# Kernel tuning notes

Measured on AMD Instinct MI355X. Metric: run time of the kernel, lower is better.

Reference implementation:

```python
import jax, jax.numpy as jnp
import numpy as np

B, L, D = 2, 2048, 1024
DH = 64
NH = D // DH
EPS = 1e-5
NEG = -1e30


def rms_norm(x, w):
    # x: (..., dh); norm in fp32 like the torch module, then scale by weight
    xf = x.astype(jnp.float32)
    y = xf * jax.lax.rsqrt(jnp.mean(xf * xf, axis=-1, keepdims=True) + EPS)
    return y.astype(x.dtype) * w.astype(x.dtype)


def sdpa(q, k, v, m):
    # q:(b,h,lq,dh) k,v:(b,h,lk,dh) m:(lq,lk) bool
    scale = 1.0 / jnp.sqrt(jnp.asarray(DH, q.dtype))
    s = jnp.einsum('bhqd,bhkd->bhqk', q, k) * scale
    s = jnp.where(m[None, None], s, NEG)
    p = jax.nn.softmax(s, axis=-1)
    return jnp.einsum('bhqk,bhkd->bhqd', p, v)


def setup_inputs() -> dict:
    key = jax.random.key(0)
    k1, k2, k3 = jax.random.split(key, 3)
    x = jax.random.normal(k1, (B, L, D), dtype=jnp.float32)
    mask = jnp.tril(jnp.ones((L, L), dtype=bool))  # causal: no fully-masked rows
    w_qkv = jax.random.normal(k2, (3 * D, D), dtype=jnp.float32) * (1.0 / np.sqrt(D))
    w_fc = jax.random.normal(k3, (D, D), dtype=jnp.float32) * (1.0 / np.sqrt(D))
    q_norm_w = jnp.ones((DH,), dtype=jnp.float32)
    k_norm_w = jnp.ones((DH,), dtype=jnp.float32)
    return {"x": x, "mask": mask, "w_qkv": w_qkv, "w_fc": w_fc,
            "q_norm_w": q_norm_w, "k_norm_w": k_norm_w,
            "subset_attention_size": 1024}


def reference(x, mask, w_qkv, w_fc, q_norm_w, k_norm_w, subset_attention_size):
    b, l, d = x.shape
    qkv = jnp.einsum('bld,ed->ble', x, w_qkv)  # (b,l,3d)
    q, k, v = jnp.split(qkv, 3, axis=-1)

    def heads(t):
        return t.reshape(b, l, NH, DH).transpose(0, 2, 1, 3)  # (b,nh,l,dh)

    q, k, v = heads(q), heads(k), heads(v)
    q = rms_norm(q, q_norm_w)
    k = rms_norm(k, k_norm_w)

    S = subset_attention_size
    if S is not None and S < l:
        o1 = sdpa(q[:, :, :S], k[:, :, :S], v[:, :, :S], mask[:S, :S])
        o2 = sdpa(q[:, :, S:], k, v, mask[S:, :])
        o = jnp.concatenate([o1, o2], axis=2)
    else:
        o = sdpa(q, k, v, mask)
    o = o.transpose(0, 2, 1, 3).reshape(b, l, d)  # (b,l,d)
    return jnp.einsum('bld,ed->ble', o, w_fc)
```

## Files before the change

### kernel.cpp

```cpp
#include <hip/hip_runtime.h>

typedef __bf16 bf16x8 __attribute__((ext_vector_type(8)));
typedef __bf16 bf16x4 __attribute__((ext_vector_type(4)));
typedef float f32x4 __attribute__((ext_vector_type(4)));
typedef short s16x4 __attribute__((ext_vector_type(4)));
typedef unsigned short u16;
typedef unsigned int u32;
typedef unsigned short u16x4 __attribute__((ext_vector_type(4)));
typedef unsigned short u16x8 __attribute__((ext_vector_type(8)));

#define AS1 __attribute__((address_space(1)))
#define AS3 __attribute__((address_space(3)))

__device__ __forceinline__ u16 f2bf(float f) {
  unsigned u = __builtin_bit_cast(unsigned, f);
  u += 0x7fffu + ((u >> 16) & 1u);
  return (u16)(u >> 16);
}

__device__ __forceinline__ float fast_exp2(float x) {
#if __has_builtin(__builtin_amdgcn_exp2f)
  return __builtin_amdgcn_exp2f(x);
#else
  return exp2f(x);
#endif
}

__device__ __forceinline__ f32x4 mfma16(s16x4 a, s16x4 b, f32x4 c) {
#if __has_builtin(__builtin_amdgcn_mfma_f32_16x16x16bf16_1k)
  return __builtin_amdgcn_mfma_f32_16x16x16bf16_1k(a, b, c, 0, 0, 0);
#else
  asm("v_mfma_f32_16x16x16_bf16 %0, %1, %2, %0" : "+v"(c) : "v"(a), "v"(b));
  return c;
#endif
}

__global__ __launch_bounds__(256) void cvt_all(const float* __restrict__ x,
                                               const float* __restrict__ wq,
                                               const float* __restrict__ wf,
                                               u16* __restrict__ xb, u16* __restrict__ wqb,
                                               u16* __restrict__ wfb) {
  long i = ((long)blockIdx.x * 256 + threadIdx.x) * 4;
  const float* src;
  u16* dst;
  long off;
  if (i < 4194304L) {
    src = x; dst = xb; off = i;
  } else if (i < 7340032L) {
    src = wq; dst = wqb; off = i - 4194304L;
  } else {
    src = wf; dst = wfb; off = i - 7340032L;
  }
  float4 v = *reinterpret_cast<const float4*>(src + off);
  u16x4 o;
  o.x = f2bf(v.x); o.y = f2bf(v.y); o.z = f2bf(v.z); o.w = f2bf(v.w);
  *reinterpret_cast<u16x4*>(dst + off) = o;
}

__global__ __launch_bounds__(256, 2) void gemm_qkv(const u16* __restrict__ A,
                                                   const u16* __restrict__ W,
                                                   u16* __restrict__ Qb,
                                                   u16* __restrict__ Kbf,
                                                   u16* __restrict__ vt,
                                                   const float* __restrict__ qw,
                                                   const float* __restrict__ kw) {
  constexpr int K = 1024;
  __shared__ __align__(16) u16 As[128 * 32];
  __shared__ __align__(16) u16 Bs[128 * 32];
  __shared__ __align__(16) u16 Ts[128 * 136];
  const int tid = threadIdx.x;
  const int lane = tid & 63;
  const int wid = tid >> 6;
  const int wm = wid >> 1, wn = wid & 1;
  const int l16 = lane & 15, g4 = lane >> 4;
  const long bm = blockIdx.x, bn = blockIdx.y;

  const int srow = tid >> 2;
  const int scol = (tid & 3) * 8;
  const u16* aA0 = A + (bm * 128 + srow) * (long)K + scol;
  const u16* aA1 = aA0 + 64 * (long)K;
  const u16* aW0 = W + (bn * 128 + srow) * (long)K + scol;
  const u16* aW1 = aW0 + 64 * (long)K;

  f32x4 acc[4][4] = {};

  for (int kt = 0; kt < K; kt += 32) {
    __builtin_amdgcn_global_load_lds((AS1 void*)(aA0 + kt), (AS3 void*)(&As[tid * 8]), 16, 0, 0);
    __builtin_amdgcn_global_load_lds((AS1 void*)(aA1 + kt), (AS3 void*)(&As[2048 + tid * 8]), 16, 0, 0);
    __builtin_amdgcn_global_load_lds((AS1 void*)(aW0 + kt), (AS3 void*)(&Bs[tid * 8]), 16, 0, 0);
    __builtin_amdgcn_global_load_lds((AS1 void*)(aW1 + kt), (AS3 void*)(&Bs[2048 + tid * 8]), 16, 0, 0);
    __syncthreads();
    bf16x8 af[4], bfr[4];
#pragma unroll
    for (int m = 0; m < 4; ++m)
      af[m] = *reinterpret_cast<const bf16x8*>(&As[(wm * 64 + m * 16 + l16) * 32 + g4 * 8]);
#pragma unroll
    for (int n = 0; n < 4; ++n)
      bfr[n] = *reinterpret_cast<const bf16x8*>(&Bs[(wn * 64 + n * 16 + l16) * 32 + g4 * 8]);
#pragma unroll
    for (int m = 0; m < 4; ++m)
#pragma unroll
      for (int n = 0; n < 4; ++n)
        acc[m][n] = __builtin_amdgcn_mfma_f32_16x16x32_bf16(af[m], bfr[n], acc[m][n], 0, 0, 0);
    __syncthreads();
  }

  if (bn < 16) {
    const float qscale = 0.18033688011112042f;
    const float* w = (bn < 8) ? qw : kw;
    const float ws = (bn < 8) ? qscale : 1.0f;
    float wv[4];
#pragma unroll
    for (int n = 0; n < 4; ++n) wv[n] = w[n * 16 + l16] * ws;
#pragma unroll
    for (int m = 0; m < 4; ++m) {
#pragma unroll
      for (int j = 0; j < 4; ++j) {
        float ss = 0.f;
#pragma unroll
        for (int n = 0; n < 4; ++n) ss = fmaf(acc[m][n][j], acc[m][n][j], ss);
        ss += __shfl_xor(ss, 1);
        ss += __shfl_xor(ss, 2);
        ss += __shfl_xor(ss, 4);
        ss += __shfl_xor(ss, 8);
        const float inv = rsqrtf(ss * (1.0f / 64.0f) + 1e-5f);
#pragma unroll
        for (int n = 0; n < 4; ++n) acc[m][n][j] *= inv * wv[n];
      }
    }
    u16* dst = (bn < 8) ? Qb : Kbf;
    const long cb = (bn < 8) ? bn : (bn - 8);
#pragma unroll
    for (int m = 0; m < 4; ++m)
#pragma unroll
      for (int n = 0; n < 4; ++n)
#pragma unroll
        for (int j = 0; j < 4; ++j) {
          long row = bm * 128 + wm * 64 + m * 16 + g4 * 4 + j;
          long col = cb * 128 + wn * 64 + n * 16 + l16;
          dst[row * 1024 + col] = f2bf(acc[m][n][j]);
        }
  } else {
#pragma unroll
    for (int m = 0; m < 4; ++m)
#pragma unroll
      for (int n = 0; n < 4; ++n) {
        bf16x4 w4;
#pragma unroll
        for (int j = 0; j < 4; ++j) w4[j] = (__bf16)acc[m][n][j];
        const int lc = wn * 64 + n * 16 + l16;
        const int lr = wm * 64 + m * 16 + g4 * 4;
        *reinterpret_cast<bf16x4*>(&Ts[lc * 136 + lr]) = w4;
      }
    __syncthreads();
    const int b = (int)(bm >> 4);
    const int keybase = ((int)(bm & 15)) * 128;
#pragma unroll
    for (int u = 0; u < 2; ++u) {
      const int unit = u * 256 + tid;
      const int hh = unit >> 8;
      const int d = (unit >> 2) & 63;
      const int kc = (unit & 3) * 32;
      const long bhv = b * 16 + (bn - 16) * 2 + hh;
      u16* dstp = vt + bhv * 131072L + (long)d * 2048 + keybase + kc;
      const u16* srcp = &Ts[(hh * 64 + d) * 136 + kc];
#pragma unroll
      for (int c = 0; c < 4; ++c)
        *reinterpret_cast<u16x8*>(dstp + c * 8) =
            *reinterpret_cast<const u16x8*>(srcp + c * 8);
    }
  }
}

__global__ __launch_bounds__(256, 2) void gemm_fc(const u16* __restrict__ A,
                                                  const u16* __restrict__ W,
                                                  float* __restrict__ C) {
  constexpr int N = 1024, K = 1024;
  __shared__ __align__(16) u16 As[128 * 32];
  __shared__ __align__(16) u16 Bs[64 * 32];
  const int tid = threadIdx.x;
  const int lane = tid & 63;
  const int wid = tid >> 6;
  const int wm = wid >> 1, wn = wid & 1;
  const int l16 = lane & 15, g4 = lane >> 4;
  const long bm = blockIdx.x, bn = blockIdx.y;

  const int srow = tid >> 2;
  const int scol = (tid & 3) * 8;
  const u16* aA0 = A + (bm * 128 + srow) * (long)K + scol;
  const u16* aA1 = aA0 + 64 * (long)K;
  const u16* aW0 = W + (bn * 64 + srow) * (long)K + scol;

  f32x4 acc[4][2] = {};

  for (int kt = 0; kt < K; kt += 32) {
    __builtin_amdgcn_global_load_lds((AS1 void*)(aA0 + kt), (AS3 void*)(&As[tid * 8]), 16, 0, 0);
    __builtin_amdgcn_global_load_lds((AS1 void*)(aA1 + kt), (AS3 void*)(&As[2048 + tid * 8]), 16, 0, 0);
    __builtin_amdgcn_global_load_lds((AS1 void*)(aW0 + kt), (AS3 void*)(&Bs[tid * 8]), 16, 0, 0);
    __syncthreads();
    bf16x8 af[4], bfr[2];
#pragma unroll
    for (int m = 0; m < 4; ++m)
      af[m] = *reinterpret_cast<const bf16x8*>(&As[(wm * 64 + m * 16 + l16) * 32 + g4 * 8]);
#pragma unroll
    for (int n = 0; n < 2; ++n)
      bfr[n] = *reinterpret_cast<const bf16x8*>(&Bs[(wn * 32 + n * 16 + l16) * 32 + g4 * 8]);
#pragma unroll
    for (int m = 0; m < 4; ++m)
#pragma unroll
      for (int n = 0; n < 2; ++n)
        acc[m][n] = __builtin_amdgcn_mfma_f32_16x16x32_bf16(af[m], bfr[n], acc[m][n], 0, 0, 0);
    __syncthreads();
  }

#pragma unroll
  for (int m = 0; m < 4; ++m)
#pragma unroll
    for (int n = 0; n < 2; ++n)
#pragma unroll
      for (int j = 0; j < 4; ++j) {
        long row = bm * 128 + wm * 64 + m * 16 + g4 * 4 + j;
        long col = bn * 64 + wn * 32 + n * 16 + l16;
        C[row * N + col] = acc[m][n][j];
      }
}

__global__ __launch_bounds__(256, 4) void attn_causal(const u16* __restrict__ Qb,
                                                      const u16* __restrict__ Kbf,
                                                      const u16* __restrict__ vt,
                                                      u16* __restrict__ o) {
  __shared__ __align__(16) u16 SMEM[16384];

  const int tid = threadIdx.x, lane = tid & 63, wid = tid >> 6;
  const int l16 = lane & 15, g4 = lane >> 4;
  const int h8 = (l16 & 7) << 4;
  const int qh = wid & 1, kh = wid >> 1;

  const int f = blockIdx.x;
  const int xcd = f & 7;
  const int g = f >> 3;
  const int hb = g >> 5;
  const int w = g & 31;
  const int bh = xcd * 4 + hb;
  const int basei = (w & 1) ? (31 - (w >> 1)) : (w >> 1);
  const int it = (hb & 1) ? (31 - basei) : basei;

  const long base = (long)(bh >> 4) * 2048 * 1024 + (bh & 15) * 64;
  const u16* qb = Qb + base;
  const u16* kb = Kbf + base;
  const u16* vtb = vt + (long)bh * 131072;

  bf16x8 qv[2][2];
#pragma unroll
  for (int qf = 0; qf < 2; ++qf) {
    const u16* qp = qb + ((long)it * 64 + qh * 32 + qf * 16 + l16) * 1024;
    qv[qf][0] = *reinterpret_cast<const bf16x8*>(qp + g4 * 8);
    qv[qf][1] = *reinterpret_cast<const bf16x8*>(qp + 32 + g4 * 8);
  }

  f32x4 acc[2][4] = {};
  f32x4 lacc[2] = {};

  s16x4 ones4;
#pragma unroll
  for (int j = 0; j < 4; ++j) ones4[j] = (short)0x3F80;

  const int krow = tid >> 3;
  const int scolE = (((tid & 7) * 16) ^ ((krow & 7) << 4)) >> 1;

  auto stage_issue = [&](int buf, int kt) {
    u16* KB = SMEM + buf * 4096;
    u16* VB = SMEM + 8192 + buf * 4096;
    __builtin_amdgcn_global_load_lds((AS1 void*)(kb + (long)(kt * 64 + krow) * 1024 + scolE),
                                     (AS3 void*)(&KB[tid * 8]), 16, 0, 0);
    __builtin_amdgcn_global_load_lds((AS1 void*)(kb + (long)(kt * 64 + krow + 32) * 1024 + scolE),
                                     (AS3 void*)(&KB[2048 + tid * 8]), 16, 0, 0);
    __builtin_amdgcn_global_load_lds((AS1 void*)(vtb + (long)krow * 2048 + kt * 64 + scolE),
                                     (AS3 void*)(&VB[tid * 8]), 16, 0, 0);
    __builtin_amdgcn_global_load_lds((AS1 void*)(vtb + (long)(krow + 32) * 2048 + kt * 64 + scolE),
                                     (AS3 void*)(&VB[2048 + tid * 8]), 16, 0, 0);
  };

  auto tile_step = [&](int cur, bool diag) {
    if (diag && qh == 0 && kh == 1) return;
    const u16* KB = SMEM + cur * 4096;
    const u16* VB = SMEM + 8192 + cur * 4096;
    bf16x8 kfr[2][2];
#pragma unroll
    for (int kf = 0; kf < 2; ++kf) {
      const int row = kh * 32 + kf * 16 + l16;
#pragma unroll
      for (int ck = 0; ck < 2; ++ck)
        kfr[kf][ck] = *reinterpret_cast<const bf16x8*>(
            &KB[row * 64 + (((ck * 64 + g4 * 16) ^ h8) >> 1)]);
    }
    f32x4 s[2][2];
    __builtin_amdgcn_s_setprio(1);
#pragma unroll
    for (int kf = 0; kf < 2; ++kf)
#pragma unroll
      for (int qf = 0; qf < 2; ++qf) {
        f32x4 z = {0.f, 0.f, 0.f, 0.f};
        z = __builtin_amdgcn_mfma_f32_16x16x32_bf16(kfr[kf][0], qv[qf][0], z, 0, 0, 0);
        z = __builtin_amdgcn_mfma_f32_16x16x32_bf16(kfr[kf][1], qv[qf][1], z, 0, 0, 0);
        s[kf][qf] = z;
      }
    __builtin_amdgcn_s_setprio(0);
    if (diag) {
#pragma unroll
      for (int kf = 0; kf < 2; ++kf)
#pragma unroll
        for (int qf = 0; qf < 2; ++qf) {
          const int keyl = kh * 32 + kf * 16 + g4 * 4;
          const int ql = qh * 32 + qf * 16 + l16;
#pragma unroll
          for (int j = 0; j < 4; ++j)
            if (keyl + j > ql) s[kf][qf][j] = -3e38f;
        }
    }
    s16x4 pfr[2][2];
#pragma unroll
    for (int kf = 0; kf < 2; ++kf)
#pragma unroll
      for (int qf = 0; qf < 2; ++qf) {
        bf16x4 p;
#pragma unroll
        for (int j = 0; j < 4; ++j) p[j] = (__bf16)fast_exp2(s[kf][qf][j]);
        pfr[kf][qf] = __builtin_bit_cast(s16x4, p);
      }
    __builtin_amdgcn_s_setprio(1);
#pragma unroll
    for (int qf = 0; qf < 2; ++qf) {
      lacc[qf] = mfma16(pfr[0][qf], ones4, lacc[qf]);
      lacc[qf] = mfma16(pfr[1][qf], ones4, lacc[qf]);
    }
#pragma unroll
    for (int db = 0; db < 4; ++db) {
      const int vrow = db * 16 + l16;
#pragma unroll
      for (int kf = 0; kf < 2; ++kf) {
        const u16x4 vv = *reinterpret_cast<const u16x4*>(
            &VB[vrow * 64 + (((kh * 64 + kf * 32 + g4 * 8) ^ h8) >> 1)]);
        const s16x4 vf = __builtin_bit_cast(s16x4, vv);
#pragma unroll
        for (int qf = 0; qf < 2; ++qf) acc[qf][db] = mfma16(pfr[kf][qf], vf, acc[qf][db]);
      }
    }
    __builtin_amdgcn_s_setprio(0);
  };

  stage_issue(0, 0);

  for (int kt = 0; kt < it; ++kt) {
    const int cur = kt & 1;
    stage_issue(cur ^ 1, kt + 1);
    asm volatile("s_waitcnt vmcnt(4)" ::: "memory");
    __builtin_amdgcn_s_barrier();
    tile_step(cur, false);
    __builtin_amdgcn_s_barrier();
  }
  asm volatile("s_waitcnt vmcnt(0)" ::: "memory");
  __builtin_amdgcn_s_barrier();
  tile_step(it & 1, true);
  __syncthreads();

  float* Ebuf = reinterpret_cast<float*>(SMEM);
  const int ebase = qh * 2176;
  if (kh == 1) {
#pragma unroll
    for (int qf = 0; qf < 2; ++qf) {
#pragma unroll
      for (int db = 0; db < 4; ++db)
#pragma unroll
        for (int j = 0; j < 4; ++j)
          Ebuf[ebase + (qf * 16 + g4 * 4 + j) * 68 + db * 16 + l16] = acc[qf][db][j];
      if (l16 == 0) {
#pragma unroll
        for (int j = 0; j < 4; ++j)
          Ebuf[ebase + (qf * 16 + g4 * 4 + j) * 68 + 64] = lacc[qf][j];
      }
    }
  }
  __syncthreads();
  if (kh == 0) {
    const long obase = (long)(bh >> 4) * 2048 * 1024 + (bh & 15) * 64;
#pragma unroll
    for (int qf = 0; qf < 2; ++qf) {
      float linv[4];
#pragma unroll
      for (int j = 0; j < 4; ++j) {
        const float lsum = lacc[qf][j] + Ebuf[ebase + (qf * 16 + g4 * 4 + j) * 68 + 64];
        linv[j] = 1.0f / lsum;
      }
#pragma unroll
      for (int db = 0; db < 4; ++db)
#pragma unroll
        for (int j = 0; j < 4; ++j) {
          const int row = qh * 32 + qf * 16 + g4 * 4 + j;
          const float v =
              acc[qf][db][j] + Ebuf[ebase + (qf * 16 + g4 * 4 + j) * 68 + db * 16 + l16];
          o[obase + ((long)it * 64 + row) * 1024 + db * 16 + l16] = f2bf(v * linv[j]);
        }
    }
  }
}

extern "C" void kernel_launch(void* const* d_in, const int* in_sizes, int n_in,
                              void* d_out, int out_size, void* d_ws, size_t ws_size,
                              hipStream_t stream) {
  const float* x = (const float*)d_in[0];
  const float* w_qkv = (const float*)d_in[2];
  const float* w_fc = (const float*)d_in[3];
  const float* qw = (const float*)d_in[4];
  const float* kw = (const float*)d_in[5];
  float* out = (float*)d_out;

  char* ws = (char*)d_ws;
  u16* xb    = (u16*)(ws);
  u16* wqkvb = (u16*)(ws + (8L << 20));
  u16* wfcb  = (u16*)(ws + (14L << 20));
  u16* Qb    = (u16*)(ws + (16L << 20));
  u16* Kbf   = (u16*)(ws + (24L << 20));
  u16* vt    = (u16*)(ws + (32L << 20));
  u16* ob    = (u16*)(ws + (40L << 20));

  cvt_all<<<8192, 256, 0, stream>>>(x, w_qkv, w_fc, xb, wqkvb, wfcb);
  gemm_qkv<<<dim3(32, 24), 256, 0, stream>>>(xb, wqkvb, Qb, Kbf, vt, qw, kw);
  attn_causal<<<1024, 256, 0, stream>>>(Qb, Kbf, vt, ob);
  gemm_fc<<<dim3(32, 16), 256, 0, stream>>>(ob, wfcb, out);
}
```

Baseline: 98.76 us.

## Software-pipeline QK of next tile with PV of current tile in attention loop

Splits the per-tile attention step into separate QK and PV phases and staggers them, so the QK MFMAs for tile i+1 are issued alongside the exp and PV work for tile i. K and V staging are decoupled, with K prefetched one tile further ahead than V. The aim is to let the two MFMA chains and the exp work interleave instead of stalling on a serial dependency. In exchange it keeps an extra score tile live in registers and makes the slot and wait-count bookkeeping more delicate.

```diff
diff --git a/kernel.cpp b/kernel.cpp
--- a/kernel.cpp
+++ b/kernel.cpp
@@ -250,14 +250,6 @@
   const u16* kb = Kbf + base;
   const u16* vtb = vt + (long)bh * 131072;
 
-  bf16x8 qv[2][2];
-#pragma unroll
-  for (int qf = 0; qf < 2; ++qf) {
-    const u16* qp = qb + ((long)it * 64 + qh * 32 + qf * 16 + l16) * 1024;
-    qv[qf][0] = *reinterpret_cast<const bf16x8*>(qp + g4 * 8);
-    qv[qf][1] = *reinterpret_cast<const bf16x8*>(qp + 32 + g4 * 8);
-  }
-
   f32x4 acc[2][4] = {};
   f32x4 lacc[2] = {};
 
@@ -268,23 +260,34 @@
   const int krow = tid >> 3;
   const int scolE = (((tid & 7) * 16) ^ ((krow & 7) << 4)) >> 1;
 
-  auto stage_issue = [&](int buf, int kt) {
-    u16* KB = SMEM + buf * 4096;
-    u16* VB = SMEM + 8192 + buf * 4096;
-    __builtin_amdgcn_global_load_lds((AS1 void*)(kb + (long)(kt * 64 + krow) * 1024 + scolE),
+  auto stage_K = [&](int tile, int slot) {
+    u16* KB = SMEM + slot * 4096;
+    __builtin_amdgcn_global_load_lds((AS1 void*)(kb + (long)(tile * 64 + krow) * 1024 + scolE),
                                      (AS3 void*)(&KB[tid * 8]), 16, 0, 0);
-    __builtin_amdgcn_global_load_lds((AS1 void*)(kb + (long)(kt * 64 + krow + 32) * 1024 + scolE),
+    __builtin_amdgcn_global_load_lds((AS1 void*)(kb + (long)(tile * 64 + krow + 32) * 1024 + scolE),
                                      (AS3 void*)(&KB[2048 + tid * 8]), 16, 0, 0);
-    __builtin_amdgcn_global_load_lds((AS1 void*)(vtb + (long)krow * 2048 + kt * 64 + scolE),
+  };
+  auto stage_V = [&](int tile, int slot) {
+    u16* VB = SMEM + 8192 + slot * 4096;
+    __builtin_amdgcn_global_load_lds((AS1 void*)(vtb + (long)krow * 2048 + tile * 64 + scolE),
                                      (AS3 void*)(&VB[tid * 8]), 16, 0, 0);
-    __builtin_amdgcn_global_load_lds((AS1 void*)(vtb + (long)(krow + 32) * 2048 + kt * 64 + scolE),
+    __builtin_amdgcn_global_load_lds((AS1 void*)(vtb + (long)(krow + 32) * 2048 + tile * 64 + scolE),
                                      (AS3 void*)(&VB[2048 + tid * 8]), 16, 0, 0);
   };
 
-  auto tile_step = [&](int cur, bool diag) {
-    if (diag && qh == 0 && kh == 1) return;
-    const u16* KB = SMEM + cur * 4096;
-    const u16* VB = SMEM + 8192 + cur * 4096;
+  bf16x8 qv[2][2];
+
+  auto qk_step = [&](f32x4 (&s)[2][2], int slot, bool diag) {
+    if (diag && qh == 0 && kh == 1) {
+#pragma unroll
+      for (int kf = 0; kf < 2; ++kf)
+#pragma unroll
+        for (int qf = 0; qf < 2; ++qf)
+#pragma unroll
+          for (int j = 0; j < 4; ++j) s[kf][qf][j] = -3e38f;
+      return;
+    }
+    const u16* KB = SMEM + slot * 4096;
     bf16x8 kfr[2][2];
 #pragma unroll
     for (int kf = 0; kf < 2; ++kf) {
@@ -294,7 +297,6 @@
         kfr[kf][ck] = *reinterpret_cast<const bf16x8*>(
             &KB[row * 64 + (((ck * 64 + g4 * 16) ^ h8) >> 1)]);
     }
-    f32x4 s[2][2];
     __builtin_amdgcn_s_setprio(1);
 #pragma unroll
     for (int kf = 0; kf < 2; ++kf)
@@ -318,6 +320,10 @@
             if (keyl + j > ql) s[kf][qf][j] = -3e38f;
         }
     }
+  };
+
+  auto pv_step = [&](const f32x4 (&s)[2][2], int slot) {
+    const u16* VB = SMEM + 8192 + slot * 4096;
     s16x4 pfr[2][2];
 #pragma unroll
     for (int kf = 0; kf < 2; ++kf)
@@ -349,19 +355,40 @@
     __builtin_amdgcn_s_setprio(0);
   };
 
-  stage_issue(0, 0);
-
-  for (int kt = 0; kt < it; ++kt) {
-    const int cur = kt & 1;
-    stage_issue(cur ^ 1, kt + 1);
+  stage_K(0, 0);
+  stage_V(0, 0);
+  stage_K(it >= 1 ? 1 : 0, 1);
+  asm volatile("s_waitcnt vmcnt(2)" ::: "memory");
+  __builtin_amdgcn_s_barrier();
+
+#pragma unroll
+  for (int qf = 0; qf < 2; ++qf) {
+    const u16* qp = qb + ((long)it * 64 + qh * 32 + qf * 16 + l16) * 1024;
+    qv[qf][0] = *reinterpret_cast<const bf16x8*>(qp + g4 * 8);
+    qv[qf][1] = *reinterpret_cast<const bf16x8*>(qp + 32 + g4 * 8);
+  }
+
+  f32x4 sA[2][2];
+  qk_step(sA, 0, it == 0);
+
+  for (int i = 0; i < it; ++i) {
+    const int si = i & 1, sn = si ^ 1;
+    stage_K(i + 2 <= it ? i + 2 : it, si);
+    stage_V(i + 1, sn);
     asm volatile("s_waitcnt vmcnt(4)" ::: "memory");
     __builtin_amdgcn_s_barrier();
-    tile_step(cur, false);
+    f32x4 sB[2][2];
+    qk_step(sB, sn, (i + 1) == it);
+    pv_step(sA, si);
+#pragma unroll
+    for (int kf = 0; kf < 2; ++kf)
+#pragma unroll
+      for (int qf = 0; qf < 2; ++qf) sA[kf][qf] = sB[kf][qf];
     __builtin_amdgcn_s_barrier();
   }
   asm volatile("s_waitcnt vmcnt(0)" ::: "memory");
   __builtin_amdgcn_s_barrier();
-  tile_step(it & 1, true);
+  pv_step(sA, it & 1);
   __syncthreads();
 
   float* Ebuf = reinterpret_cast<float*>(SMEM);
```

Measured after the change: 100.9 us. +2.2%, slower.
